# Performance work log

Measured on AMD Instinct MI355X. Metric: run time of the kernel, lower is better.

Reference implementation:

```python
import jax, jax.numpy as jnp
import numpy as np

NUM_EMB = 1024
EMB_DIM = 256
COMM_COST = 0.25
BETA = 0.25


def setup_inputs() -> dict:
    key = jax.random.key(0)
    k1, k2 = jax.random.split(key)
    x = jax.random.normal(k1, (16, EMB_DIM, 64, 64), dtype=jnp.float32)
    # nn.Embedding initialized uniform(-1/num_emb, 1/num_emb)
    emb_weight = jax.random.uniform(
        k2, (NUM_EMB, EMB_DIM), dtype=jnp.float32,
        minval=-1.0 / NUM_EMB, maxval=1.0 / NUM_EMB)
    return {"x": x, "emb_weight": emb_weight}


def reference(x, emb_weight):
    # x: [B, C, H, W] -> [B, H, W, C]
    xp = jnp.transpose(x, (0, 2, 3, 1))
    B, H, W, C = xp.shape
    flat = xp.reshape(-1, C)  # [N, C]
    # squared euclidean distances (argmin-equivalent to torch.cdist)
    d2 = (jnp.sum(flat * flat, axis=1, keepdims=True)
          - 2.0 * jnp.einsum('nc,kc->nk', flat, emb_weight)
          + jnp.sum(emb_weight * emb_weight, axis=1))  # [N, K]
    idx = jnp.argmin(d2, axis=1)  # [N]
    quantized = emb_weight[idx].reshape(B, H, W, C)
    e_latent_loss = jnp.mean((jax.lax.stop_gradient(quantized) - xp) ** 2) * BETA
    q_latent_loss = jnp.mean((quantized - jax.lax.stop_gradient(xp)) ** 2)
    c_loss = q_latent_loss + COMM_COST * e_latent_loss
    # straight-through estimator
    quant_st = xp + jax.lax.stop_gradient(quantized - xp)
    quant_out = jnp.transpose(quant_st, (0, 3, 1, 2))  # [B, C, H, W]
    return (c_loss, quant_out)
```

## Files before the change

### kernel.cpp

```cpp
#include <hip/hip_runtime.h>
#include <hip/hip_bf16.h>
#include <cstdint>
#include <cstddef>

#define EMB_K   1024
#define EMB_C   256
#define HWB     4096
#define NPIX    65536

typedef __bf16 bf16x8 __attribute__((ext_vector_type(8)));
typedef float  f32x4  __attribute__((ext_vector_type(4)));

__device__ __forceinline__ unsigned short bf16bits(float v) {
  __hip_bfloat16 h = __float2bfloat16(v);
  return __builtin_bit_cast(unsigned short, h);
}

__global__ void k_emb(const float* __restrict__ emb, unsigned short* __restrict__ emb_bf,
                      float* __restrict__ enorm, float* __restrict__ loss) {
  int k = blockIdx.x;
  int c = threadIdx.x;
  if (k == 0 && c == 0) *loss = 0.f;
  float v = emb[(size_t)k * EMB_C + c];
  int kt = k >> 6, g2 = (k >> 4) & 3, lr = k & 15;
  int s = c >> 5, quad = (c >> 3) & 3, j = c & 7;
  size_t chunk = (size_t)kt * 2048 + (size_t)((g2 * 8 + s) * 64 + quad * 16 + lr);
  emb_bf[chunk * 8 + j] = bf16bits(v);
  float sq = v * v;
  for (int m = 32; m; m >>= 1) sq += __shfl_down(sq, m, 64);
  __shared__ float red[4];
  int lane = c & 63, w = c >> 6;
  if (lane == 0) red[w] = sq;
  __syncthreads();
  if (c == 0) enorm[k] = red[0] + red[1] + red[2] + red[3];
}

__device__ __forceinline__ void stage64(const unsigned short* __restrict__ tile_src,
                                        unsigned char* buf, int t) {
#pragma unroll
  for (int j = 0; j < 4; ++j) {
    int d = j * 512 + t;
    __builtin_amdgcn_global_load_lds(
        (const __attribute__((address_space(1))) void*)(tile_src + (size_t)d * 8),
        (__attribute__((address_space(3))) void*)(buf + (unsigned)(j * 8192 + (t >> 6) * 1024)),
        16, 0, 0);
  }
}

__device__ __forceinline__ int posA(int cc, int nl) {
  return ((cc >> 3) << 3) | ((cc & 7) ^ ((nl ^ (nl >> 2)) & 7));
}

#define LDS_BYTES 141376

__global__ __launch_bounds__(512) void
k_main(const float* __restrict__ x, const unsigned short* __restrict__ embbf,
       const float* __restrict__ enorm, unsigned* __restrict__ keys_g,
       float* __restrict__ loss) {
  extern __shared__ char smem[];
  unsigned char* Abase = (unsigned char*)smem + 65536;
  float*    cjl    = (float*)(smem + 131072);
  unsigned* keys_l = (unsigned*)(smem + 135168);
  float*    xn_l   = (float*)(smem + 136192);
  float*    xn_p   = (float*)(smem + 137216);
  float*    red    = (float*)(smem + 141312);

  int n0 = blockIdx.x * 256;
  int b  = n0 >> 12, hw0 = n0 & 4095;
  int t = threadIdx.x, w = t >> 6, lane = t & 63;
  int quad = lane >> 4, lr = lane & 15;
  int g  = w >> 1;
  int h2 = w & 1;

  stage64(embbf,          (unsigned char*)smem,         t);
  stage64(embbf + 16384,  (unsigned char*)smem + 32768, t);

  if (t < 256) keys_l[t] = 0u;
  for (int i = t; i < 1024; i += 512) cjl[i] = 0.375f - 0.5f * enorm[i];
  __syncthreads();

  bf16x8 af[4][8];
#pragma unroll
  for (int p = 0; p < 2; ++p) {
    if (p) __syncthreads();
    int hwq = t & 31;
    int cg  = t >> 5;
    float xn[4] = {0.f, 0.f, 0.f, 0.f};
    {
      const float* xp = x + (size_t)b * (EMB_C * HWB) + hw0 + p * 128 + hwq * 4;
      f32x4 v16[16];
#pragma unroll
      for (int j = 0; j < 16; ++j)
        v16[j] = *(const f32x4*)(xp + (size_t)(cg * 16 + j) * HWB);
      unsigned pk[4][8] = {};
#pragma unroll
      for (int j = 0; j < 16; ++j)
#pragma unroll
        for (int m = 0; m < 4; ++m) {
          xn[m] += v16[j][m] * v16[j][m];
          pk[m][j >> 1] |= (unsigned)bf16bits(v16[j][m]) << ((j & 1) * 16);
        }
#pragma unroll
      for (int m = 0; m < 4; ++m) {
        int nl = hwq * 4 + m;
        *(uint4*)(Abase + nl * 512 + posA(cg * 2,     nl) * 16) = *(const uint4*)&pk[m][0];
        *(uint4*)(Abase + nl * 512 + posA(cg * 2 + 1, nl) * 16) = *(const uint4*)&pk[m][4];
      }
    }
#pragma unroll
    for (int m = 0; m < 4; ++m) xn[m] += __shfl_xor(xn[m], 32, 64);
    if (lane < 32) {
#pragma unroll
      for (int m = 0; m < 4; ++m) xn_p[w * 128 + lane * 4 + m] = xn[m];
    }
    __syncthreads();
    if (t < 128) {
      float sum = 0.f;
#pragma unroll
      for (int ww = 0; ww < 8; ++ww) sum += xn_p[ww * 128 + t];
      xn_l[p * 128 + t] = sum;
    }
    if ((g >> 1) == p) {
#pragma unroll
      for (int i = 0; i < 4; ++i) {
        int rA = (g & 1) * 64 + i * 16 + lr;
#pragma unroll
        for (int s = 0; s < 8; ++s) {
          int cc = s * 4 + quad;
          af[i][s] = *(const bf16x8*)(Abase + rA * 512 + posA(cc, rA) * 16);
        }
      }
    }
  }
  __syncthreads();

  unsigned best[4][4] = {};
  for (int kt = 0; kt < 16; ++kt) {
    if (kt < 14)
      stage64(embbf + (size_t)(kt + 2) * 16384,
              (unsigned char*)smem + (((kt + 2) & 3) << 15), t);
    if (kt < 14)       asm volatile("s_waitcnt vmcnt(8)" ::: "memory");
    else if (kt == 14) asm volatile("s_waitcnt vmcnt(4)" ::: "memory");
    else               asm volatile("s_waitcnt vmcnt(0)" ::: "memory");
    __builtin_amdgcn_s_barrier();
    __builtin_amdgcn_sched_barrier(0);
    const uint4* sb = (const uint4*)(smem + ((kt & 3) << 15));
    float cj[2]; unsigned kp[2];
#pragma unroll
    for (int j = 0; j < 2; ++j) {
      int k = kt * 64 + h2 * 32 + j * 16 + lr;
      cj[j] = cjl[k];
      kp[j] = 1023u - (unsigned)k;
    }
    f32x4 acc[4][2] = {};
#pragma unroll
    for (int s = 0; s < 8; ++s) {
      bf16x8 bf[2];
#pragma unroll
      for (int j = 0; j < 2; ++j) {
        uint4 q = sb[((h2 * 2 + j) * 8 + s) * 64 + lane];
        bf[j] = __builtin_bit_cast(bf16x8, q);
      }
#pragma unroll
      for (int i = 0; i < 4; ++i)
#pragma unroll
        for (int j = 0; j < 2; ++j)
          acc[i][j] = __builtin_amdgcn_mfma_f32_16x16x32_bf16(af[i][s], bf[j], acc[i][j], 0, 0, 0);
    }
#pragma unroll
    for (int i = 0; i < 4; ++i)
#pragma unroll
      for (int j = 0; j < 2; ++j)
#pragma unroll
        for (int r = 0; r < 4; ++r) {
          float f = acc[i][j][r] + cj[j];
          unsigned key = (__float_as_uint(f) & 0xFFFFFC00u) | kp[j];
          best[i][r] = best[i][r] > key ? best[i][r] : key;
        }
  }
  __syncthreads();

#pragma unroll
  for (int i = 0; i < 4; ++i)
#pragma unroll
    for (int r = 0; r < 4; ++r) {
      unsigned v = best[i][r];
#pragma unroll
      for (int m = 1; m < 16; m <<= 1) {
        unsigned o = (unsigned)__shfl_xor((int)v, m, 64);
        v = v > o ? v : o;
      }
      if (lr == 0) atomicMax(&keys_l[g * 64 + i * 16 + quad * 4 + r], v);
    }
  __syncthreads();

  if (t < 256) {
    unsigned key = keys_l[t];
    keys_g[n0 + t] = key;
    float fh = __uint_as_float(key & 0xFFFFFC00u);
    float lsum = xn_l[t] + 0.75f - 2.0f * fh;
    for (int m = 32; m; m >>= 1) lsum += __shfl_down(lsum, m, 64);
    if (lane == 0) red[w] = lsum;
  }
  __syncthreads();
  if (t == 0)
    atomicAdd(loss, red[0] + red[1] + red[2] + red[3]);
}

__global__ __launch_bounds__(256) void
k_out(const float* __restrict__ emb, const unsigned* __restrict__ keys_g,
      const float* __restrict__ loss, float* __restrict__ out) {
  __shared__ float tile[64 * 68];
  __shared__ int   idx_l[64];
  int e  = blockIdx.x;
  int nt = e >> 1, cH = e & 1;
  int n0 = nt * 64;
  int b  = n0 >> 12, hw0 = n0 & 4095;
  int t = threadIdx.x, w = t >> 6, lane = t & 63;
  if (e == 0 && t == 0)
    out[0] = 1.0625f * (*loss) / 16777216.0f;
  if (t < 64) idx_l[t] = 1023 - (int)(keys_g[n0 + t] & 1023u);
  __syncthreads();
  int nn = t >> 2, ch = t & 3;
  int nrot = (nn - 3) & 63;
  const float* er = emb + (size_t)idx_l[nn] * EMB_C + cH * 128;
  float* ob = out + 1 + (size_t)b * (EMB_C * HWB) + (size_t)cH * 128 * HWB + hw0;
  for (int p = 0; p < 2; ++p) {
    if (p) __syncthreads();
#pragma unroll
    for (int q = 0; q < 4; ++q) {
      f32x4 v = *(const f32x4*)(er + p * 64 + q * 16 + ch * 4);
#pragma unroll
      for (int m = 0; m < 4; ++m)
        tile[(q * 16 + ch * 4 + m) * 68 + nrot] = v[m];
    }
    __syncthreads();
#pragma unroll
    for (int cc = 0; cc < 4; ++cc) {
      int cl = w * 16 + cc * 4 + (lane >> 4);
      int i  = lane & 15;
      const float* tr = tile + cl * 68;
      float* F = ob + (size_t)(p * 64 + cl) * HWB;
      if (i < 15) {
        f32x4 qv = *(const f32x4*)(tr + 4 * i);
        *(f32x4*)(F + 3 + 4 * i) = qv;
      } else {
        F[0] = tr[61]; F[1] = tr[62]; F[2] = tr[63];
        F[63] = tr[60];
      }
    }
  }
}

extern "C" void kernel_launch(void* const* d_in, const int* in_sizes, int n_in,
                              void* d_out, int out_size, void* d_ws, size_t ws_size,
                              hipStream_t stream) {
  const float* x   = (const float*)d_in[0];
  const float* emb = (const float*)d_in[1];
  float* out = (float*)d_out;
  char*  ws  = (char*)d_ws;

  unsigned short* emb_bf = (unsigned short*)ws;
  float*          enorm  = (float*)(ws + 524288);
  float*          loss   = (float*)(ws + 528384);
  unsigned*       keys_g = (unsigned*)(ws + 532480);

  hipFuncSetAttribute((const void*)k_main,
                      hipFuncAttributeMaxDynamicSharedMemorySize, LDS_BYTES);

  k_emb <<<dim3(EMB_K),      dim3(EMB_C), 0,         stream>>>(emb, emb_bf, enorm, loss);
  k_main<<<dim3(NPIX / 256), dim3(512),   LDS_BYTES, stream>>>(x, emb_bf, enorm,
                                                               keys_g, loss);
  k_out <<<dim3(NPIX / 32),  dim3(256),   0,         stream>>>(emb, keys_g, loss, out);
}
```

Baseline: 151.7 us.

## Remap warp tiling to 128 rows by 16 codes per wave

Changes the per-wave tile from 64 pixel rows by 32 codebook entries to 128 rows by 16 entries, so each wave keeps eight A fragments (64 bf16x8 registers) and loads one B fragment per k-step instead of two. This halves LDS reads of codebook data per MFMA but doubles the A-fragment register footprint and accumulator count per wave, which raises register pressure and may reduce occupancy or cause spills. The reduction indexing is updated to match the new 2x4 wave layout.

```diff
diff --git a/kernel.cpp b/kernel.cpp
--- a/kernel.cpp
+++ b/kernel.cpp
@@ -69,8 +69,8 @@
   int b  = n0 >> 12, hw0 = n0 & 4095;
   int t = threadIdx.x, w = t >> 6, lane = t & 63;
   int quad = lane >> 4, lr = lane & 15;
-  int g  = w >> 1;
-  int h2 = w & 1;
+  int g  = w >> 2;
+  int h4 = w & 3;
 
   stage64(embbf,          (unsigned char*)smem,         t);
   stage64(embbf + 16384,  (unsigned char*)smem + 32768, t);
@@ -79,7 +79,7 @@
   for (int i = t; i < 1024; i += 512) cjl[i] = 0.375f - 0.5f * enorm[i];
   __syncthreads();
 
-  bf16x8 af[4][8];
+  bf16x8 af[8][8];
 #pragma unroll
   for (int p = 0; p < 2; ++p) {
     if (p) __syncthreads();
@@ -120,10 +120,10 @@
       for (int ww = 0; ww < 8; ++ww) sum += xn_p[ww * 128 + t];
       xn_l[p * 128 + t] = sum;
     }
-    if ((g >> 1) == p) {
-#pragma unroll
-      for (int i = 0; i < 4; ++i) {
-        int rA = (g & 1) * 64 + i * 16 + lr;
+    if (g == p) {
+#pragma unroll
+      for (int i = 0; i < 8; ++i) {
+        int rA = i * 16 + lr;
 #pragma unroll
         for (int s = 0; s < 8; ++s) {
           int cc = s * 4 + quad;
@@ -134,7 +134,7 @@
   }
   __syncthreads();
 
-  unsigned best[4][4] = {};
+  unsigned best[8][4] = {};
   for (int kt = 0; kt < 16; ++kt) {
     if (kt < 14)
       stage64(embbf + (size_t)(kt + 2) * 16384,
@@ -145,43 +145,31 @@
     __builtin_amdgcn_s_barrier();
     __builtin_amdgcn_sched_barrier(0);
     const uint4* sb = (const uint4*)(smem + ((kt & 3) << 15));
-    float cj[2]; unsigned kp[2];
-#pragma unroll
-    for (int j = 0; j < 2; ++j) {
-      int k = kt * 64 + h2 * 32 + j * 16 + lr;
-      cj[j] = cjl[k];
-      kp[j] = 1023u - (unsigned)k;
-    }
-    f32x4 acc[4][2] = {};
+    int k = kt * 64 + h4 * 16 + lr;
+    float cj = cjl[k];
+    unsigned kp = 1023u - (unsigned)k;
+    f32x4 acc[8] = {};
 #pragma unroll
     for (int s = 0; s < 8; ++s) {
-      bf16x8 bf[2];
-#pragma unroll
-      for (int j = 0; j < 2; ++j) {
-        uint4 q = sb[((h2 * 2 + j) * 8 + s) * 64 + lane];
-        bf[j] = __builtin_bit_cast(bf16x8, q);
-      }
-#pragma unroll
-      for (int i = 0; i < 4; ++i)
-#pragma unroll
-        for (int j = 0; j < 2; ++j)
-          acc[i][j] = __builtin_amdgcn_mfma_f32_16x16x32_bf16(af[i][s], bf[j], acc[i][j], 0, 0, 0);
-    }
-#pragma unroll
-    for (int i = 0; i < 4; ++i)
-#pragma unroll
-      for (int j = 0; j < 2; ++j)
-#pragma unroll
-        for (int r = 0; r < 4; ++r) {
-          float f = acc[i][j][r] + cj[j];
-          unsigned key = (__float_as_uint(f) & 0xFFFFFC00u) | kp[j];
-          best[i][r] = best[i][r] > key ? best[i][r] : key;
-        }
-  }
-  __syncthreads();
-
-#pragma unroll
-  for (int i = 0; i < 4; ++i)
+      uint4 q = sb[(h4 * 8 + s) * 64 + lane];
+      bf16x8 bf = __builtin_bit_cast(bf16x8, q);
+#pragma unroll
+      for (int i = 0; i < 8; ++i)
+        acc[i] = __builtin_amdgcn_mfma_f32_16x16x32_bf16(af[i][s], bf, acc[i], 0, 0, 0);
+    }
+#pragma unroll
+    for (int i = 0; i < 8; ++i)
+#pragma unroll
+      for (int r = 0; r < 4; ++r) {
+        float f = acc[i][r] + cj;
+        unsigned key = (__float_as_uint(f) & 0xFFFFFC00u) | kp;
+        best[i][r] = best[i][r] > key ? best[i][r] : key;
+      }
+  }
+  __syncthreads();
+
+#pragma unroll
+  for (int i = 0; i < 8; ++i)
 #pragma unroll
     for (int r = 0; r < 4; ++r) {
       unsigned v = best[i][r];
@@ -190,7 +178,7 @@
         unsigned o = (unsigned)__shfl_xor((int)v, m, 64);
         v = v > o ? v : o;
       }
-      if (lr == 0) atomicMax(&keys_l[g * 64 + i * 16 + quad * 4 + r], v);
+      if (lr == 0) atomicMax(&keys_l[g * 128 + i * 16 + quad * 4 + r], v);
     }
   __syncthreads();
 
```

Result: slower. 272.5 us (+79.6%).
